# Kernel tuning notes

Measured on AMD Instinct MI355X. Metric: run time of the kernel, lower is better.

## Reference

```python
import jax, jax.numpy as jnp
import numpy as np

N_NODES = 100000
N_EDGES = 1600000
D_IN, D_HID, N_CLASS = 256, 64, 40


def setup_inputs() -> dict:
    key = jax.random.key(0)
    ks = jax.random.split(key, 8)
    x = jax.random.normal(ks[0], (N_NODES, D_IN), dtype=jnp.float32)
    edge_src = jax.random.randint(ks[1], (N_EDGES,), 0, N_NODES, dtype=jnp.int64)
    edge_dst = jax.random.randint(ks[2], (N_EDGES,), 0, N_NODES, dtype=jnp.int64)
    edge_weight = jax.random.uniform(ks[3], (N_EDGES,), dtype=jnp.float32)
    W1 = jax.random.normal(ks[4], (D_IN, D_HID), dtype=jnp.float32) * (1.0 / np.sqrt(D_IN))
    b1 = jnp.zeros((D_HID,), dtype=jnp.float32)
    W2 = jax.random.normal(ks[5], (D_HID, N_CLASS), dtype=jnp.float32) * (1.0 / np.sqrt(D_HID))
    b2 = jnp.zeros((N_CLASS,), dtype=jnp.float32)
    return {"x": x, "edge_src": edge_src, "edge_dst": edge_dst,
            "edge_weight": edge_weight, "W1": W1, "b1": b1, "W2": W2, "b2": b2}


def _gcn_layer(h, W, b, edge_src, edge_dst, edge_weight):
    # support = h @ W  (dense transform), then sparse adj matmul:
    # out[dst] += w * support[src]
    support = h @ W                              # [N, d_out]
    msgs = edge_weight[:, None] * support[edge_src]  # [E, d_out] gather
    agg = jax.ops.segment_sum(msgs, edge_dst, num_segments=N_NODES)
    return agg + b


def reference(x, edge_src, edge_dst, edge_weight, W1, b1, W2, b2):
    # dropout prob = 0.0 -> identity (deterministic reference)
    h = _gcn_layer(x, W1, b1, edge_src, edge_dst, edge_weight)
    h = _gcn_layer(h, W2, b2, edge_src, edge_dst, edge_weight)
    return jax.nn.log_softmax(h, axis=1)
```

## Files before the change

kernel.cpp:

```cpp
#include <hip/hip_runtime.h>
#include <hip/hip_bf16.h>
#include <math.h>

#define N_NODES 100000
#define N_EDGES 1600000
#define D_IN    256
#define D_HID   64
#define N_CLASS 40

#define SCAN_CHUNK 256
#define SCAN_NB    ((N_NODES + SCAN_CHUNK - 1) / SCAN_CHUNK)
#define SLOT_MAX   48
#define GEMM_NB    ((N_NODES + 255) / 256)
#define FILL_NB    ((N_EDGES + 255) / 256)

__global__ __launch_bounds__(256) void prep_kernel(
    const float* __restrict__ W1, const float* __restrict__ W2,
    const float* __restrict__ b1, float* __restrict__ W12t, float* __restrict__ c1)
{
    int idx = blockIdx.x * 256 + threadIdx.x;
    if (idx < D_IN * N_CLASS) {
        int k = idx / N_CLASS;
        int c = idx - k * N_CLASS;
        float s = 0.f;
#pragma unroll
        for (int j = 0; j < D_HID; ++j)
            s = fmaf(W1[k * D_HID + j], W2[j * N_CLASS + c], s);
        W12t[c * D_IN + k] = s;
    }
    if (blockIdx.x == 0 && threadIdx.x < N_CLASS) {
        int c = threadIdx.x;
        float s = 0.f;
#pragma unroll
        for (int j = 0; j < D_HID; ++j)
            s = fmaf(b1[j], W2[j * N_CLASS + c], s);
        c1[c] = s;
    }
}

__device__ __forceinline__ void gemm_body(
    int gblk, int tid,
    const float* __restrict__ x, const float* __restrict__ W12t,
    float* __restrict__ T, float* xs, float* wt)
{
    const int row0 = gblk * 256;

    for (int i = tid; i < N_CLASS * D_IN; i += 256) {
        int c = i >> 8;
        int k = i & 255;
        wt[c * 260 + k] = W12t[i];
    }

    const int rg = tid >> 2;
    const int cg = tid & 3;
    const int c0 = cg * 10;

    float acc[4][10];
#pragma unroll
    for (int r = 0; r < 4; ++r)
#pragma unroll
        for (int j = 0; j < 10; ++j) acc[r][j] = 0.f;

    const float4* x4 = (const float4*)x;
    float4* xs4 = (float4*)xs;
    const float4* wt4 = (const float4*)wt;

    for (int kb = 0; kb < 8; ++kb) {
        __syncthreads();
#pragma unroll
        for (int ph = 0; ph < 8; ++ph) {
            int i = ph * 256 + tid;
            int r  = i >> 3;
            int c4 = i & 7;
            int grow = min(row0 + r, N_NODES - 1);
            float4 v = x4[(size_t)grow * 64 + kb * 8 + c4];
            xs4[r * 8 + (c4 ^ ((r >> 2) & 7))] = v;
        }
        __syncthreads();

#pragma unroll
        for (int k4 = 0; k4 < 8; ++k4) {
            float4 xv[4];
#pragma unroll
            for (int r = 0; r < 4; ++r)
                xv[r] = xs4[(rg * 4 + r) * 8 + (k4 ^ (rg & 7))];
#pragma unroll
            for (int j = 0; j < 10; ++j) {
                float4 w = wt4[(c0 + j) * 65 + kb * 8 + k4];
#pragma unroll
                for (int r = 0; r < 4; ++r)
                    acc[r][j] = fmaf(xv[r].x, w.x,
                                fmaf(xv[r].y, w.y,
                                fmaf(xv[r].z, w.z,
                                fmaf(xv[r].w, w.w, acc[r][j]))));
            }
        }
    }

#pragma unroll
    for (int r = 0; r < 4; ++r) {
        int row = row0 + rg * 4 + r;
        if (row < N_NODES) {
            size_t ob = (size_t)row * N_CLASS + c0;
#pragma unroll
            for (int j = 0; j < 10; ++j) T[ob + j] = acc[r][j];
        }
    }
}

__global__ __launch_bounds__(256) void gemm_fill_kernel(
    const float* __restrict__ x, const float* __restrict__ W12t,
    float* __restrict__ T,
    const int* __restrict__ esrc, const int* __restrict__ edst,
    const float* __restrict__ ew, int* __restrict__ cnt,
    int2* __restrict__ slots)
{
    __shared__ float xs[256 * 32];
    __shared__ float wt[N_CLASS * 260];
    const int tid = threadIdx.x;

    if (blockIdx.x < GEMM_NB) {
        gemm_body(blockIdx.x, tid, x, W12t, T, xs, wt);
    } else {
        int e = (blockIdx.x - GEMM_NB) * 256 + tid;
        if (e < N_EDGES) {
            int d = edst[e];
            int slot = atomicAdd(&cnt[d], 1);
            if (slot < SLOT_MAX)
                slots[(size_t)d * SLOT_MAX + slot] =
                    make_int2(esrc[e], __float_as_int(ew[e]));
        }
    }
}

__global__ __launch_bounds__(256) void gemm_t_kernel(
    const float* __restrict__ x, const float* __restrict__ W12t,
    float* __restrict__ T)
{
    __shared__ float xs[256 * 32];
    __shared__ float wt[N_CLASS * 260];
    gemm_body(blockIdx.x, threadIdx.x, x, W12t, T, xs, wt);
}

__global__ __launch_bounds__(256) void hist_kernel(
    const int* __restrict__ edst, int* __restrict__ cnt)
{
    int e = blockIdx.x * 256 + threadIdx.x;
    if (e >= N_EDGES) return;
    atomicAdd(&cnt[edst[e]], 1);
}

__global__ __launch_bounds__(256) void scan_partial_kernel(
    const int* __restrict__ cnt, int* __restrict__ bsum)
{
    __shared__ int red[256];
    int t = threadIdx.x;
    int idx = blockIdx.x * SCAN_CHUNK + t;
    int v = (idx < N_NODES) ? cnt[idx] : 0;
    red[t] = v;
    __syncthreads();
#pragma unroll
    for (int off = 128; off > 0; off >>= 1) {
        if (t < off) red[t] += red[t + off];
        __syncthreads();
    }
    if (t == 0) bsum[blockIdx.x] = red[0];
}

__global__ __launch_bounds__(512) void scan_block_kernel(
    const int* __restrict__ bsum, int* __restrict__ boff)
{
    __shared__ int s[512];
    int t = threadIdx.x;
    int v = (t < SCAN_NB) ? bsum[t] : 0;
    s[t] = v;
    __syncthreads();
#pragma unroll
    for (int off = 1; off < 512; off <<= 1) {
        int u = (t >= off) ? s[t - off] : 0;
        __syncthreads();
        s[t] += u;
        __syncthreads();
    }
    if (t < SCAN_NB) boff[t] = s[t] - v;
}

__global__ __launch_bounds__(256) void scan_final_kernel(
    const int* __restrict__ cnt, const int* __restrict__ boff,
    int* __restrict__ row_ptr)
{
    __shared__ int s[256];
    int t = threadIdx.x;
    int idx = blockIdx.x * SCAN_CHUNK + t;
    int v = (idx < N_NODES) ? cnt[idx] : 0;
    s[t] = v;
    __syncthreads();
#pragma unroll
    for (int off = 1; off < 256; off <<= 1) {
        int u = (t >= off) ? s[t - off] : 0;
        __syncthreads();
        s[t] += u;
        __syncthreads();
    }
    if (idx < N_NODES) row_ptr[idx] = boff[blockIdx.x] + s[t] - v;
}

__global__ __launch_bounds__(256) void fill_kernel(
    const int* __restrict__ esrc, const int* __restrict__ edst,
    const float* __restrict__ ew, int* __restrict__ row_ptr,
    int2* __restrict__ edges_s)
{
    int e = blockIdx.x * 256 + threadIdx.x;
    if (e >= N_EDGES) return;
    int d = edst[e];
    int pos = atomicAdd(&row_ptr[d], 1);
    edges_s[pos] = make_int2(esrc[e], __float_as_int(ew[e]));
}

template<bool SLOTS, bool SMAX>
__global__ __launch_bounds__(256) void agg_kernel(
    const int2* __restrict__ edges_s, const int* __restrict__ meta,
    const float* __restrict__ Tin, float* __restrict__ Tout,
    const float* __restrict__ c1, const float* __restrict__ b2)
{
    __shared__ float red[25][11];
    __shared__ float wsh[25];
    const int t = threadIdx.x;
    const int nl  = t / 10;
    const int sub = t % 10;
    const int node = blockIdx.x * 25 + nl;
    const bool active = (t < 250) && (node < N_NODES);

    int beg = 0, end = 0;
    if (active) {
        if (SLOTS) {
            beg = node * SLOT_MAX;
            int c = meta[node];
            end = beg + (c > SLOT_MAX ? SLOT_MAX : c);
        } else {
            beg = node ? meta[node - 1] : 0;
            end = meta[node];
        }
    }

    const float4* Tin4 = (const float4*)Tin;
    float4 acc = make_float4(0.f, 0.f, 0.f, 0.f);
    float wsum = 0.f;

    int e = beg;
    for (; e + 3 < end; e += 4) {
        int2 a0 = edges_s[e];
        int2 a1 = edges_s[e + 1];
        int2 a2 = edges_s[e + 2];
        int2 a3 = edges_s[e + 3];
        float4 v0 = Tin4[a0.x * 10 + sub];
        float4 v1 = Tin4[a1.x * 10 + sub];
        float4 v2 = Tin4[a2.x * 10 + sub];
        float4 v3 = Tin4[a3.x * 10 + sub];
        float w0 = __int_as_float(a0.y), w1 = __int_as_float(a1.y);
        float w2 = __int_as_float(a2.y), w3 = __int_as_float(a3.y);
        acc.x = fmaf(w0, v0.x, acc.x); acc.y = fmaf(w0, v0.y, acc.y);
        acc.z = fmaf(w0, v0.z, acc.z); acc.w = fmaf(w0, v0.w, acc.w);
        acc.x = fmaf(w1, v1.x, acc.x); acc.y = fmaf(w1, v1.y, acc.y);
        acc.z = fmaf(w1, v1.z, acc.z); acc.w = fmaf(w1, v1.w, acc.w);
        acc.x = fmaf(w2, v2.x, acc.x); acc.y = fmaf(w2, v2.y, acc.y);
        acc.z = fmaf(w2, v2.z, acc.z); acc.w = fmaf(w2, v2.w, acc.w);
        acc.x = fmaf(w3, v3.x, acc.x); acc.y = fmaf(w3, v3.y, acc.y);
        acc.z = fmaf(w3, v3.z, acc.z); acc.w = fmaf(w3, v3.w, acc.w);
        if (SMAX) wsum += (w0 + w1) + (w2 + w3);
    }
    for (; e < end; ++e) {
        int2 a0 = edges_s[e];
        float w0 = __int_as_float(a0.y);
        float4 v0 = Tin4[a0.x * 10 + sub];
        acc.x = fmaf(w0, v0.x, acc.x); acc.y = fmaf(w0, v0.y, acc.y);
        acc.z = fmaf(w0, v0.z, acc.z); acc.w = fmaf(w0, v0.w, acc.w);
        if (SMAX) wsum += w0;
    }

    if (!SMAX) {
        if (active) ((float4*)Tout)[(size_t)node * 10 + sub] = acc;
        return;
    }

    if (active && sub == 0) wsh[nl] = wsum;
    __syncthreads();
    float dw = active ? wsh[nl] : 0.f;

    float4 cv = ((const float4*)c1)[sub];
    float4 bv = ((const float4*)b2)[sub];
    float4 z;
    z.x = fmaf(dw, cv.x, acc.x + bv.x);
    z.y = fmaf(dw, cv.y, acc.y + bv.y);
    z.z = fmaf(dw, cv.z, acc.z + bv.z);
    z.w = fmaf(dw, cv.w, acc.w + bv.w);

    float m4 = fmaxf(fmaxf(z.x, z.y), fmaxf(z.z, z.w));
    if (active) red[nl][sub] = m4;
    __syncthreads();
    float m = -INFINITY;
    if (active)
#pragma unroll
        for (int j = 0; j < 10; ++j) m = fmaxf(m, red[nl][j]);
    __syncthreads();

    float s4 = expf(z.x - m) + expf(z.y - m) + expf(z.z - m) + expf(z.w - m);
    if (active) red[nl][sub] = s4;
    __syncthreads();
    if (active) {
        float s = 0.f;
#pragma unroll
        for (int j = 0; j < 10; ++j) s += red[nl][j];
        float ls = m + logf(s);
        float4 o;
        o.x = z.x - ls; o.y = z.y - ls; o.z = z.z - ls; o.w = z.w - ls;
        ((float4*)Tout)[(size_t)node * 10 + sub] = o;
    }
}

extern "C" void kernel_launch(void* const* d_in, const int* in_sizes, int n_in,
                              void* d_out, int out_size, void* d_ws, size_t ws_size,
                              hipStream_t stream)
{
    const float* x    = (const float*)d_in[0];
    const int*   esrc = (const int*)  d_in[1];
    const int*   edst = (const int*)  d_in[2];
    const float* ew   = (const float*)d_in[3];
    const float* W1   = (const float*)d_in[4];
    const float* b1   = (const float*)d_in[5];
    const float* W2   = (const float*)d_in[6];
    const float* b2   = (const float*)d_in[7];
    float* out = (float*)d_out;

    char* ws = (char*)d_ws;
    const size_t SLOTS_BYTES = (size_t)N_NODES * SLOT_MAX * 8;
    const size_t NEED_SLOTS  = SLOTS_BYTES + 32000000 + 1000000;
    const bool use_slots = (ws_size >= NEED_SLOTS);

    if (use_slots) {
        int2*  slots = (int2*) (ws);
        float* T     = (float*)(ws + SLOTS_BYTES);
        float* Y1    = (float*)(ws + SLOTS_BYTES + 16000000);
        int*   cnt   = (int*)  (ws + SLOTS_BYTES + 32000000);
        float* W12t  = (float*)(ws + SLOTS_BYTES + 32400000);
        float* c1    = (float*)(ws + SLOTS_BYTES + 32441984);

        hipMemsetAsync(cnt, 0, 400000, stream);
        prep_kernel<<<(D_IN * N_CLASS + 255) / 256, 256, 0, stream>>>(W1, W2, b1, W12t, c1);
        gemm_fill_kernel<<<GEMM_NB + FILL_NB, 256, 0, stream>>>(
            x, W12t, T, esrc, edst, ew, cnt, slots);
        agg_kernel<true, false><<<(N_NODES + 24) / 25, 256, 0, stream>>>(
            slots, cnt, T, Y1, nullptr, nullptr);
        agg_kernel<true, true><<<(N_NODES + 24) / 25, 256, 0, stream>>>(
            slots, cnt, Y1, out, c1, b2);
    } else {
        float* T       = (float*)(ws);
        float* Y1      = (float*)(ws + 16000000);
        int2*  edges_s = (int2*) (ws + 32000000);
        int*   row_ptr = (int*)  (ws + 44800000);
        int*   cnt     = (int*)  (ws + 45200016);
        float* W12t    = (float*)(ws + 45600016);
        float* c1      = (float*)(ws + 45640976);
        int*   bsum    = (int*)  (ws + 45641200);
        int*   boff    = (int*)  (ws + 45642800);

        hipMemsetAsync(cnt, 0, 400000, stream);
        prep_kernel<<<(D_IN * N_CLASS + 255) / 256, 256, 0, stream>>>(W1, W2, b1, W12t, c1);
        gemm_t_kernel<<<GEMM_NB, 256, 0, stream>>>(x, W12t, T);
        hist_kernel<<<FILL_NB, 256, 0, stream>>>(edst, cnt);
        scan_partial_kernel<<<SCAN_NB, 256, 0, stream>>>(cnt, bsum);
        scan_block_kernel<<<1, 512, 0, stream>>>(bsum, boff);
        scan_final_kernel<<<SCAN_NB, 256, 0, stream>>>(cnt, boff, row_ptr);
        fill_kernel<<<FILL_NB, 256, 0, stream>>>(esrc, edst, ew, row_ptr, edges_s);
        agg_kernel<false, false><<<(N_NODES + 24) / 25, 256, 0, stream>>>(
            edges_s, row_ptr, T, Y1, nullptr, nullptr);
        agg_kernel<false, true><<<(N_NODES + 24) / 25, 256, 0, stream>>>(
            edges_s, row_ptr, Y1, out, c1, b2);
    }
}
```

Baseline: 382.3 us.

## Drop shared W12t staging, read weights wave-uniformly from global, grid-stride edge fill

The GEMM no longer copies the 40x256 combined weight into shared memory. Each wavefront now owns 10 output columns, with the column index made uniform via readfirstlane, so the weight loads become scalar/broadcast global reads. This frees about 41KB of LDS per block, and launch bounds request 4 blocks per CU to raise occupancy. The fused edge-fill part now uses a fixed 1024-block grid-stride loop, which shrinks the fused grid but does more work per thread.

```diff
diff --git a/kernel.cpp b/kernel.cpp
--- a/kernel.cpp
+++ b/kernel.cpp
@@ -12,7 +12,8 @@
 #define SCAN_NB    ((N_NODES + SCAN_CHUNK - 1) / SCAN_CHUNK)
 #define SLOT_MAX   48
 #define GEMM_NB    ((N_NODES + 255) / 256)
-#define FILL_NB    ((N_EDGES + 255) / 256)
+#define FILL_NB    1024
+#define EDGE_NB    ((N_EDGES + 255) / 256)
 
 __global__ __launch_bounds__(256) void prep_kernel(
     const float* __restrict__ W1, const float* __restrict__ W2,
@@ -41,19 +42,11 @@
 __device__ __forceinline__ void gemm_body(
     int gblk, int tid,
     const float* __restrict__ x, const float* __restrict__ W12t,
-    float* __restrict__ T, float* xs, float* wt)
+    float* __restrict__ T, float* xs)
 {
     const int row0 = gblk * 256;
-
-    for (int i = tid; i < N_CLASS * D_IN; i += 256) {
-        int c = i >> 8;
-        int k = i & 255;
-        wt[c * 260 + k] = W12t[i];
-    }
-
-    const int rg = tid >> 2;
-    const int cg = tid & 3;
-    const int c0 = cg * 10;
+    const int lane = tid & 63;
+    const int c0 = __builtin_amdgcn_readfirstlane(tid >> 6) * 10;
 
     float acc[4][10];
 #pragma unroll
@@ -61,15 +54,15 @@
 #pragma unroll
         for (int j = 0; j < 10; ++j) acc[r][j] = 0.f;
 
-    const float4* x4 = (const float4*)x;
-    float4* xs4 = (float4*)xs;
-    const float4* wt4 = (const float4*)wt;
+    const float4* x4  = (const float4*)x;
+    float4*       xs4 = (float4*)xs;
+    const float4* w4  = (const float4*)W12t;
 
     for (int kb = 0; kb < 8; ++kb) {
         __syncthreads();
 #pragma unroll
         for (int ph = 0; ph < 8; ++ph) {
-            int i = ph * 256 + tid;
+            int i  = ph * 256 + tid;
             int r  = i >> 3;
             int c4 = i & 7;
             int grow = min(row0 + r, N_NODES - 1);
@@ -83,10 +76,10 @@
             float4 xv[4];
 #pragma unroll
             for (int r = 0; r < 4; ++r)
-                xv[r] = xs4[(rg * 4 + r) * 8 + (k4 ^ (rg & 7))];
+                xv[r] = xs4[(lane * 4 + r) * 8 + (k4 ^ (lane & 7))];
 #pragma unroll
             for (int j = 0; j < 10; ++j) {
-                float4 w = wt4[(c0 + j) * 65 + kb * 8 + k4];
+                float4 w = w4[(c0 + j) * 64 + kb * 8 + k4];
 #pragma unroll
                 for (int r = 0; r < 4; ++r)
                     acc[r][j] = fmaf(xv[r].x, w.x,
@@ -99,7 +92,7 @@
 
 #pragma unroll
     for (int r = 0; r < 4; ++r) {
-        int row = row0 + rg * 4 + r;
+        int row = row0 + lane * 4 + r;
         if (row < N_NODES) {
             size_t ob = (size_t)row * N_CLASS + c0;
 #pragma unroll
@@ -108,7 +101,7 @@
     }
 }
 
-__global__ __launch_bounds__(256) void gemm_fill_kernel(
+__global__ __launch_bounds__(256, 4) void gemm_fill_kernel(
     const float* __restrict__ x, const float* __restrict__ W12t,
     float* __restrict__ T,
     const int* __restrict__ esrc, const int* __restrict__ edst,
@@ -116,30 +109,30 @@
     int2* __restrict__ slots)
 {
     __shared__ float xs[256 * 32];
-    __shared__ float wt[N_CLASS * 260];
     const int tid = threadIdx.x;
 
     if (blockIdx.x < GEMM_NB) {
-        gemm_body(blockIdx.x, tid, x, W12t, T, xs, wt);
+        gemm_body(blockIdx.x, tid, x, W12t, T, xs);
     } else {
-        int e = (blockIdx.x - GEMM_NB) * 256 + tid;
-        if (e < N_EDGES) {
-            int d = edst[e];
+        const int e0 = (blockIdx.x - GEMM_NB) * 256 + tid;
+        for (int e = e0; e < N_EDGES; e += FILL_NB * 256) {
+            int   d = edst[e];
+            int   s = esrc[e];
+            float w = ew[e];
             int slot = atomicAdd(&cnt[d], 1);
             if (slot < SLOT_MAX)
                 slots[(size_t)d * SLOT_MAX + slot] =
-                    make_int2(esrc[e], __float_as_int(ew[e]));
-        }
-    }
-}
-
-__global__ __launch_bounds__(256) void gemm_t_kernel(
+                    make_int2(s, __float_as_int(w));
+        }
+    }
+}
+
+__global__ __launch_bounds__(256, 4) void gemm_t_kernel(
     const float* __restrict__ x, const float* __restrict__ W12t,
     float* __restrict__ T)
 {
     __shared__ float xs[256 * 32];
-    __shared__ float wt[N_CLASS * 260];
-    gemm_body(blockIdx.x, threadIdx.x, x, W12t, T, xs, wt);
+    gemm_body(blockIdx.x, threadIdx.x, x, W12t, T, xs);
 }
 
 __global__ __launch_bounds__(256) void hist_kernel(
@@ -367,11 +360,11 @@
         hipMemsetAsync(cnt, 0, 400000, stream);
         prep_kernel<<<(D_IN * N_CLASS + 255) / 256, 256, 0, stream>>>(W1, W2, b1, W12t, c1);
         gemm_t_kernel<<<GEMM_NB, 256, 0, stream>>>(x, W12t, T);
-        hist_kernel<<<FILL_NB, 256, 0, stream>>>(edst, cnt);
+        hist_kernel<<<EDGE_NB, 256, 0, stream>>>(edst, cnt);
         scan_partial_kernel<<<SCAN_NB, 256, 0, stream>>>(cnt, bsum);
         scan_block_kernel<<<1, 512, 0, stream>>>(bsum, boff);
         scan_final_kernel<<<SCAN_NB, 256, 0, stream>>>(cnt, boff, row_ptr);
-        fill_kernel<<<FILL_NB, 256, 0, stream>>>(esrc, edst, ew, row_ptr, edges_s);
+        fill_kernel<<<EDGE_NB, 256, 0, stream>>>(esrc, edst, ew, row_ptr, edges_s);
         agg_kernel<false, false><<<(N_NODES + 24) / 25, 256, 0, stream>>>(
             edges_s, row_ptr, T, Y1, nullptr, nullptr);
         agg_kernel<false, true><<<(N_NODES + 24) / 25, 256, 0, stream>>>(
```

Measured after the change: 374.0 us. 2.2% less time.

## Partition slot fill into destination-range passes and unroll aggregation gathers by eight

Applied to the files above, without the earlier changes.

The fused gemm/fill kernel now runs a fixed grid of fill blocks that sweep all edges eight times. Each pass handles only destinations in one eighth of the node range, so the scattered atomics and slot writes stay in a smaller, more cache-resident region. The cost is reading edst eight times. The aggregation loop also gets an 8-wide unrolled batch of independent gathers to raise memory-level parallelism, at some cost in register pressure. The CSR-path launches are renamed to EDGE_NB so they keep their old grid size.

```diff
diff --git a/kernel.cpp b/kernel.cpp
--- a/kernel.cpp
+++ b/kernel.cpp
@@ -12,7 +12,10 @@
 #define SCAN_NB    ((N_NODES + SCAN_CHUNK - 1) / SCAN_CHUNK)
 #define SLOT_MAX   48
 #define GEMM_NB    ((N_NODES + 255) / 256)
-#define FILL_NB    ((N_EDGES + 255) / 256)
+#define FILL_NB    1024
+#define EDGE_NB    ((N_EDGES + 255) / 256)
+#define NPASS      8
+#define PASS_RNG   ((N_NODES + NPASS - 1) / NPASS)
 
 __global__ __launch_bounds__(256) void prep_kernel(
     const float* __restrict__ W1, const float* __restrict__ W2,
@@ -122,13 +125,19 @@
     if (blockIdx.x < GEMM_NB) {
         gemm_body(blockIdx.x, tid, x, W12t, T, xs, wt);
     } else {
-        int e = (blockIdx.x - GEMM_NB) * 256 + tid;
-        if (e < N_EDGES) {
-            int d = edst[e];
-            int slot = atomicAdd(&cnt[d], 1);
-            if (slot < SLOT_MAX)
-                slots[(size_t)d * SLOT_MAX + slot] =
-                    make_int2(esrc[e], __float_as_int(ew[e]));
+        const int b = blockIdx.x - GEMM_NB;
+        for (int p = 0; p < NPASS; ++p) {
+            const int dlo = p * PASS_RNG;
+            const int dhi = dlo + PASS_RNG;
+            for (int e = b * 256 + tid; e < N_EDGES; e += FILL_NB * 256) {
+                int d = edst[e];
+                if (d >= dlo && d < dhi) {
+                    int slot = atomicAdd(&cnt[d], 1);
+                    if (slot < SLOT_MAX)
+                        slots[(size_t)d * SLOT_MAX + slot] =
+                            make_int2(esrc[e], __float_as_int(ew[e]));
+                }
+            }
         }
     }
 }
@@ -248,33 +257,48 @@
     float wsum = 0.f;
 
     int e = beg;
+    for (; e + 7 < end; e += 8) {
+        int2 a[8];
+        float4 v[8];
+#pragma unroll
+        for (int q = 0; q < 8; ++q) a[q] = edges_s[e + q];
+#pragma unroll
+        for (int q = 0; q < 8; ++q) v[q] = Tin4[a[q].x * 10 + sub];
+#pragma unroll
+        for (int q = 0; q < 8; ++q) {
+            float w = __int_as_float(a[q].y);
+            acc.x = fmaf(w, v[q].x, acc.x);
+            acc.y = fmaf(w, v[q].y, acc.y);
+            acc.z = fmaf(w, v[q].z, acc.z);
+            acc.w = fmaf(w, v[q].w, acc.w);
+            if (SMAX) wsum += w;
+        }
+    }
     for (; e + 3 < end; e += 4) {
-        int2 a0 = edges_s[e];
-        int2 a1 = edges_s[e + 1];
-        int2 a2 = edges_s[e + 2];
-        int2 a3 = edges_s[e + 3];
-        float4 v0 = Tin4[a0.x * 10 + sub];
-        float4 v1 = Tin4[a1.x * 10 + sub];
-        float4 v2 = Tin4[a2.x * 10 + sub];
-        float4 v3 = Tin4[a3.x * 10 + sub];
-        float w0 = __int_as_float(a0.y), w1 = __int_as_float(a1.y);
-        float w2 = __int_as_float(a2.y), w3 = __int_as_float(a3.y);
-        acc.x = fmaf(w0, v0.x, acc.x); acc.y = fmaf(w0, v0.y, acc.y);
-        acc.z = fmaf(w0, v0.z, acc.z); acc.w = fmaf(w0, v0.w, acc.w);
-        acc.x = fmaf(w1, v1.x, acc.x); acc.y = fmaf(w1, v1.y, acc.y);
-        acc.z = fmaf(w1, v1.z, acc.z); acc.w = fmaf(w1, v1.w, acc.w);
-        acc.x = fmaf(w2, v2.x, acc.x); acc.y = fmaf(w2, v2.y, acc.y);
-        acc.z = fmaf(w2, v2.z, acc.z); acc.w = fmaf(w2, v2.w, acc.w);
-        acc.x = fmaf(w3, v3.x, acc.x); acc.y = fmaf(w3, v3.y, acc.y);
-        acc.z = fmaf(w3, v3.z, acc.z); acc.w = fmaf(w3, v3.w, acc.w);
-        if (SMAX) wsum += (w0 + w1) + (w2 + w3);
+        int2 a[4];
+        float4 v[4];
+#pragma unroll
+        for (int q = 0; q < 4; ++q) a[q] = edges_s[e + q];
+#pragma unroll
+        for (int q = 0; q < 4; ++q) v[q] = Tin4[a[q].x * 10 + sub];
+#pragma unroll
+        for (int q = 0; q < 4; ++q) {
+            float w = __int_as_float(a[q].y);
+            acc.x = fmaf(w, v[q].x, acc.x);
+            acc.y = fmaf(w, v[q].y, acc.y);
+            acc.z = fmaf(w, v[q].z, acc.z);
+            acc.w = fmaf(w, v[q].w, acc.w);
+            if (SMAX) wsum += w;
+        }
     }
     for (; e < end; ++e) {
         int2 a0 = edges_s[e];
         float w0 = __int_as_float(a0.y);
         float4 v0 = Tin4[a0.x * 10 + sub];
-        acc.x = fmaf(w0, v0.x, acc.x); acc.y = fmaf(w0, v0.y, acc.y);
-        acc.z = fmaf(w0, v0.z, acc.z); acc.w = fmaf(w0, v0.w, acc.w);
+        acc.x = fmaf(w0, v0.x, acc.x);
+        acc.y = fmaf(w0, v0.y, acc.y);
+        acc.z = fmaf(w0, v0.z, acc.z);
+        acc.w = fmaf(w0, v0.w, acc.w);
         if (SMAX) wsum += w0;
     }
 
@@ -367,11 +391,11 @@
         hipMemsetAsync(cnt, 0, 400000, stream);
         prep_kernel<<<(D_IN * N_CLASS + 255) / 256, 256, 0, stream>>>(W1, W2, b1, W12t, c1);
         gemm_t_kernel<<<GEMM_NB, 256, 0, stream>>>(x, W12t, T);
-        hist_kernel<<<FILL_NB, 256, 0, stream>>>(edst, cnt);
+        hist_kernel<<<EDGE_NB, 256, 0, stream>>>(edst, cnt);
         scan_partial_kernel<<<SCAN_NB, 256, 0, stream>>>(cnt, bsum);
         scan_block_kernel<<<1, 512, 0, stream>>>(bsum, boff);
         scan_final_kernel<<<SCAN_NB, 256, 0, stream>>>(cnt, boff, row_ptr);
-        fill_kernel<<<FILL_NB, 256, 0, stream>>>(esrc, edst, ew, row_ptr, edges_s);
+        fill_kernel<<<EDGE_NB, 256, 0, stream>>>(esrc, edst, ew, row_ptr, edges_s);
         agg_kernel<false, false><<<(N_NODES + 24) / 25, 256, 0, stream>>>(
             edges_s, row_ptr, T, Y1, nullptr, nullptr);
         agg_kernel<false, true><<<(N_NODES + 24) / 25, 256, 0, stream>>>(
```

Result: slower. 435.4 us (+13.9%).

## Store intermediate node features as fp16 in 128-byte padded rows

Applied to the files above, without the earlier changes.

The GEMM output T and the first aggregation output Y1 are now stored as half precision, with each row padded to 64 halves (128 bytes) so a node's row aligns to cache lines. The aggregation gathers 8-byte half4 chunks and converts them to fp32 before accumulating. The edge loop is unrolled to 8 so more gathers are in flight. This roughly halves gather traffic and the footprint of the random-access tables, at the cost of fp16 rounding on intermediate values.

```diff
diff --git a/kernel.cpp b/kernel.cpp
--- a/kernel.cpp
+++ b/kernel.cpp
@@ -1,5 +1,5 @@
 #include <hip/hip_runtime.h>
-#include <hip/hip_bf16.h>
+#include <hip/hip_fp16.h>
 #include <math.h>
 
 #define N_NODES 100000
@@ -13,6 +13,7 @@
 #define SLOT_MAX   48
 #define GEMM_NB    ((N_NODES + 255) / 256)
 #define FILL_NB    ((N_EDGES + 255) / 256)
+#define TSTRIDE    64
 
 __global__ __launch_bounds__(256) void prep_kernel(
     const float* __restrict__ W1, const float* __restrict__ W2,
@@ -41,7 +42,7 @@
 __device__ __forceinline__ void gemm_body(
     int gblk, int tid,
     const float* __restrict__ x, const float* __restrict__ W12t,
-    float* __restrict__ T, float* xs, float* wt)
+    __half* __restrict__ T, float* xs, float* wt)
 {
     const int row0 = gblk * 256;
 
@@ -101,16 +102,17 @@
     for (int r = 0; r < 4; ++r) {
         int row = row0 + rg * 4 + r;
         if (row < N_NODES) {
-            size_t ob = (size_t)row * N_CLASS + c0;
-#pragma unroll
-            for (int j = 0; j < 10; ++j) T[ob + j] = acc[r][j];
+            __half2* Trow = (__half2*)(T + (size_t)row * TSTRIDE + c0);
+#pragma unroll
+            for (int q = 0; q < 5; ++q)
+                Trow[q] = __floats2half2_rn(acc[r][2 * q], acc[r][2 * q + 1]);
         }
     }
 }
 
 __global__ __launch_bounds__(256) void gemm_fill_kernel(
     const float* __restrict__ x, const float* __restrict__ W12t,
-    float* __restrict__ T,
+    __half* __restrict__ T,
     const int* __restrict__ esrc, const int* __restrict__ edst,
     const float* __restrict__ ew, int* __restrict__ cnt,
     int2* __restrict__ slots)
@@ -124,18 +126,20 @@
     } else {
         int e = (blockIdx.x - GEMM_NB) * 256 + tid;
         if (e < N_EDGES) {
-            int d = edst[e];
+            int   d = edst[e];
+            int   s = esrc[e];
+            float w = ew[e];
             int slot = atomicAdd(&cnt[d], 1);
             if (slot < SLOT_MAX)
                 slots[(size_t)d * SLOT_MAX + slot] =
-                    make_int2(esrc[e], __float_as_int(ew[e]));
+                    make_int2(s, __float_as_int(w));
         }
     }
 }
 
 __global__ __launch_bounds__(256) void gemm_t_kernel(
     const float* __restrict__ x, const float* __restrict__ W12t,
-    float* __restrict__ T)
+    __half* __restrict__ T)
 {
     __shared__ float xs[256 * 32];
     __shared__ float wt[N_CLASS * 260];
@@ -220,7 +224,7 @@
 template<bool SLOTS, bool SMAX>
 __global__ __launch_bounds__(256) void agg_kernel(
     const int2* __restrict__ edges_s, const int* __restrict__ meta,
-    const float* __restrict__ Tin, float* __restrict__ Tout,
+    const __half* __restrict__ Tin, void* __restrict__ Tout,
     const float* __restrict__ c1, const float* __restrict__ b2)
 {
     __shared__ float red[25][11];
@@ -243,43 +247,50 @@
         }
     }
 
-    const float4* Tin4 = (const float4*)Tin;
+    const uint2* Tin8 = (const uint2*)Tin;
     float4 acc = make_float4(0.f, 0.f, 0.f, 0.f);
     float wsum = 0.f;
 
     int e = beg;
-    for (; e + 3 < end; e += 4) {
-        int2 a0 = edges_s[e];
-        int2 a1 = edges_s[e + 1];
-        int2 a2 = edges_s[e + 2];
-        int2 a3 = edges_s[e + 3];
-        float4 v0 = Tin4[a0.x * 10 + sub];
-        float4 v1 = Tin4[a1.x * 10 + sub];
-        float4 v2 = Tin4[a2.x * 10 + sub];
-        float4 v3 = Tin4[a3.x * 10 + sub];
-        float w0 = __int_as_float(a0.y), w1 = __int_as_float(a1.y);
-        float w2 = __int_as_float(a2.y), w3 = __int_as_float(a3.y);
-        acc.x = fmaf(w0, v0.x, acc.x); acc.y = fmaf(w0, v0.y, acc.y);
-        acc.z = fmaf(w0, v0.z, acc.z); acc.w = fmaf(w0, v0.w, acc.w);
-        acc.x = fmaf(w1, v1.x, acc.x); acc.y = fmaf(w1, v1.y, acc.y);
-        acc.z = fmaf(w1, v1.z, acc.z); acc.w = fmaf(w1, v1.w, acc.w);
-        acc.x = fmaf(w2, v2.x, acc.x); acc.y = fmaf(w2, v2.y, acc.y);
-        acc.z = fmaf(w2, v2.z, acc.z); acc.w = fmaf(w2, v2.w, acc.w);
-        acc.x = fmaf(w3, v3.x, acc.x); acc.y = fmaf(w3, v3.y, acc.y);
-        acc.z = fmaf(w3, v3.z, acc.z); acc.w = fmaf(w3, v3.w, acc.w);
-        if (SMAX) wsum += (w0 + w1) + (w2 + w3);
+    for (; e + 7 < end; e += 8) {
+        int2 a[8];
+        uint2 g[8];
+#pragma unroll
+        for (int q = 0; q < 8; ++q) a[q] = edges_s[e + q];
+#pragma unroll
+        for (int q = 0; q < 8; ++q) g[q] = Tin8[a[q].x * 16 + sub];
+#pragma unroll
+        for (int q = 0; q < 8; ++q) {
+            float w = __int_as_float(a[q].y);
+            float2 f0 = __half22float2(*(const __half2*)&g[q].x);
+            float2 f1 = __half22float2(*(const __half2*)&g[q].y);
+            acc.x = fmaf(w, f0.x, acc.x);
+            acc.y = fmaf(w, f0.y, acc.y);
+            acc.z = fmaf(w, f1.x, acc.z);
+            acc.w = fmaf(w, f1.y, acc.w);
+            if (SMAX) wsum += w;
+        }
     }
     for (; e < end; ++e) {
         int2 a0 = edges_s[e];
         float w0 = __int_as_float(a0.y);
-        float4 v0 = Tin4[a0.x * 10 + sub];
-        acc.x = fmaf(w0, v0.x, acc.x); acc.y = fmaf(w0, v0.y, acc.y);
-        acc.z = fmaf(w0, v0.z, acc.z); acc.w = fmaf(w0, v0.w, acc.w);
+        uint2 g0 = Tin8[a0.x * 16 + sub];
+        float2 f0 = __half22float2(*(const __half2*)&g0.x);
+        float2 f1 = __half22float2(*(const __half2*)&g0.y);
+        acc.x = fmaf(w0, f0.x, acc.x);
+        acc.y = fmaf(w0, f0.y, acc.y);
+        acc.z = fmaf(w0, f1.x, acc.z);
+        acc.w = fmaf(w0, f1.y, acc.w);
         if (SMAX) wsum += w0;
     }
 
     if (!SMAX) {
-        if (active) ((float4*)Tout)[(size_t)node * 10 + sub] = acc;
+        if (active) {
+            uint2 o;
+            *(__half2*)&o.x = __floats2half2_rn(acc.x, acc.y);
+            *(__half2*)&o.y = __floats2half2_rn(acc.z, acc.w);
+            ((uint2*)Tout)[(size_t)node * 16 + sub] = o;
+        }
         return;
     }
 
@@ -338,12 +349,12 @@
     const bool use_slots = (ws_size >= NEED_SLOTS);
 
     if (use_slots) {
-        int2*  slots = (int2*) (ws);
-        float* T     = (float*)(ws + SLOTS_BYTES);
-        float* Y1    = (float*)(ws + SLOTS_BYTES + 16000000);
-        int*   cnt   = (int*)  (ws + SLOTS_BYTES + 32000000);
-        float* W12t  = (float*)(ws + SLOTS_BYTES + 32400000);
-        float* c1    = (float*)(ws + SLOTS_BYTES + 32441984);
+        int2*   slots = (int2*)  (ws);
+        __half* T     = (__half*)(ws + SLOTS_BYTES);
+        __half* Y1    = (__half*)(ws + SLOTS_BYTES + 16000000);
+        int*    cnt   = (int*)   (ws + SLOTS_BYTES + 32000000);
+        float*  W12t  = (float*) (ws + SLOTS_BYTES + 32400000);
+        float*  c1    = (float*) (ws + SLOTS_BYTES + 32441984);
 
         hipMemsetAsync(cnt, 0, 400000, stream);
         prep_kernel<<<(D_IN * N_CLASS + 255) / 256, 256, 0, stream>>>(W1, W2, b1, W12t, c1);
@@ -354,15 +365,15 @@
         agg_kernel<true, true><<<(N_NODES + 24) / 25, 256, 0, stream>>>(
             slots, cnt, Y1, out, c1, b2);
     } else {
-        float* T       = (float*)(ws);
-        float* Y1      = (float*)(ws + 16000000);
-        int2*  edges_s = (int2*) (ws + 32000000);
-        int*   row_ptr = (int*)  (ws + 44800000);
-        int*   cnt     = (int*)  (ws + 45200016);
-        float* W12t    = (float*)(ws + 45600016);
-        float* c1      = (float*)(ws + 45640976);
-        int*   bsum    = (int*)  (ws + 45641200);
-        int*   boff    = (int*)  (ws + 45642800);
+        __half* T       = (__half*)(ws);
+        __half* Y1      = (__half*)(ws + 16000000);
+        int2*   edges_s = (int2*)  (ws + 32000000);
+        int*    row_ptr = (int*)   (ws + 44800000);
+        int*    cnt     = (int*)   (ws + 45200016);
+        float*  W12t    = (float*) (ws + 45600016);
+        float*  c1      = (float*) (ws + 45640976);
+        int*    bsum    = (int*)   (ws + 45641200);
+        int*    boff    = (int*)   (ws + 45642800);
 
         hipMemsetAsync(cnt, 0, 400000, stream);
         prep_kernel<<<(D_IN * N_CLASS + 255) / 256, 256, 0, stream>>>(W1, W2, b1, W12t, c1);
```

New measurement: 342.5 us. -10.4%, faster.
